# Kernel optimization log

Measured on AMD Instinct MI355X. Metric: run time of the kernel, lower is better.

Reference implementation:

```python
import jax, jax.numpy as jnp
import numpy as np

D = 2048  # d_model
B = 64    # batch
S = 32    # seq_len (module is designed for 32-step sequences)
C = 8     # number of control embeddings
INITRANGE = 0.1


def setup_inputs() -> dict:
    key = jax.random.key(0)
    ks = jax.random.split(key, 6)

    def lin_w(k):
        return jax.random.uniform(k, (D, D), minval=-INITRANGE, maxval=INITRANGE, dtype=jnp.float32)

    zb = jnp.zeros((D,), dtype=jnp.float32)
    return {
        "sequence": jax.random.normal(ks[0], (B, S, D), dtype=jnp.float32),
        "controls": jax.random.normal(ks[1], (C, B, D), dtype=jnp.float32),
        "Wq": lin_w(ks[2]), "bq": zb,
        "Wk": lin_w(ks[3]), "bk": zb,
        "Wv": lin_w(ks[4]), "bv": zb,
        "Wo": lin_w(ks[5]), "bo": zb,
    }


def reference(sequence, controls, Wq, bq, Wk, bk, Wv, bv, Wo, bo):
    # sequence: (B, S, D); controls: (C, B, D) = stacked list of control embeddings.
    d = sequence.shape[-1]
    queries = sequence @ Wq.T + bq            # (B, S, D)
    keys = controls @ Wk.T + bk               # (C, B, D)  == control_key(c).unsqueeze(1)
    values = controls @ Wv.T + bv             # (C, B, D)
    # bmm(queries, keys^T) with a single key per control -> scores (C, B, S, 1)
    scores = jnp.einsum('bsd,cbd->cbs', queries, keys)[..., None] / jnp.sqrt(jnp.asarray(d, sequence.dtype))
    attn = jax.nn.softmax(scores, axis=-1)    # softmax over a size-1 axis -> exactly 1.0
    attended = attn * values[:, :, None, :]   # (C, B, S, D); bmm(attn, values)
    # dropout is identity in eval mode
    projected = jnp.einsum('cbsd,ed->cbse', attended, Wo) + bo  # per-control output_proj
    # residual accumulation over the control loop == sum over C
    return sequence + projected.sum(axis=0)
```

## Files before the change

### kernel.cpp

```cpp
#include <hip/hip_runtime.h>
#include <hip/hip_bf16.h>

#define DM 2048
#define BB 64
#define SS 32
#define CC 8

typedef __attribute__((ext_vector_type(8))) short short8;
typedef __attribute__((ext_vector_type(4))) short short4v;
typedef __attribute__((ext_vector_type(4))) float f32x4;

static __device__ __forceinline__ short f2bf(float f) {
  union { __hip_bfloat16 h; short s; } u;
  u.h = __float2bfloat16(f);
  return u.s;
}

__global__ void k1_sum_bf16(const float* __restrict__ controls,
                            short* __restrict__ u16) {
  const int idx = blockIdx.x * 128 + threadIdx.x;
  const int b = idx >> 9;
  const int k = (idx & 511) * 4;
  float4 s = make_float4(0.f, 0.f, 0.f, 0.f);
#pragma unroll
  for (int c = 0; c < CC; ++c) {
    const float4 v = *reinterpret_cast<const float4*>(
        controls + ((size_t)c * BB + b) * DM + k);
    s.x += v.x; s.y += v.y; s.z += v.z; s.w += v.w;
  }
  short4v o = {f2bf(s.x), f2bf(s.y), f2bf(s.z), f2bf(s.w)};
  *reinterpret_cast<short4v*>(u16 + (size_t)b * DM + k) = o;
}

template <int EPI>
__global__ __launch_bounds__(512, 4) void gemm_full(
    const short* __restrict__ abf, const float* __restrict__ w,
    const float* __restrict__ bias, short* __restrict__ vout,
    const float* __restrict__ seq, float* __restrict__ out) {
  __shared__ float lwW[8][2][16 * 64];
  __shared__ f32x4 red[7][64];
  __shared__ float ptt[16][16];

  const int t    = threadIdx.x;
  const int lane = t & 63;
  const int wv   = t >> 6;
  const int eb   = blockIdx.x & 127;
  const int bg   = blockIdx.x >> 7;
  const int e0   = eb * 16;
  const int b0   = bg * 16;
  const int kq   = wv * 256;

  const int srow4 = lane >> 4;
  const int sg    = lane & 15;
  const int r = lane & 15, ksub = lane >> 4;

  const short* abase = abf + (size_t)(b0 + r) * DM + kq + ksub * 8;

  short8 areg[2][2];
  f32x4 acc = {0.f, 0.f, 0.f, 0.f};

#define ISSUE_W(c, bsel)                                                      \
  {                                                                           \
    const int ck = kq + (c) * 64;                                             \
    float* wd = &lwW[wv][bsel][0];                                            \
    _Pragma("unroll") for (int i = 0; i < 4; ++i) {                           \
      const int row = 4 * i + srow4;                                          \
      const float* src =                                                      \
          w + (size_t)(e0 + row) * DM + ck + ((sg ^ row) << 2);               \
      __builtin_amdgcn_global_load_lds(                                       \
          (const __attribute__((address_space(1))) void*)src,                 \
          (__attribute__((address_space(3))) void*)(wd + i * 256), 16, 0, 0); \
    }                                                                         \
  }
#define LOAD_A(c, bsel)                                                       \
  {                                                                           \
    areg[bsel][0] = *reinterpret_cast<const short8*>(abase + (c) * 64);       \
    areg[bsel][1] = *reinterpret_cast<const short8*>(abase + (c) * 64 + 32);  \
  }

  ISSUE_W(0, 0)
  LOAD_A(0, 0)

#pragma unroll
  for (int c = 0; c < 4; ++c) {
    if (c < 3) {
      ISSUE_W(c + 1, (c + 1) & 1)
      LOAD_A(c + 1, (c + 1) & 1)
      asm volatile("s_waitcnt vmcnt(6)" ::: "memory");
    } else {
      asm volatile("s_waitcnt vmcnt(0)" ::: "memory");
    }
    __builtin_amdgcn_sched_barrier(0);

    const float* wb = &lwW[wv][c & 1][0];
#pragma unroll
    for (int s = 0; s < 2; ++s) {
      const int gl = s * 8 + ksub * 2;
      const float4 lo =
          *reinterpret_cast<const float4*>(wb + r * 64 + ((gl ^ r) << 2));
      const float4 hi = *reinterpret_cast<const float4*>(
          wb + r * 64 + (((gl + 1) ^ r) << 2));
      short8 bf;
      bf[0] = f2bf(lo.x); bf[1] = f2bf(lo.y);
      bf[2] = f2bf(lo.z); bf[3] = f2bf(lo.w);
      bf[4] = f2bf(hi.x); bf[5] = f2bf(hi.y);
      bf[6] = f2bf(hi.z); bf[7] = f2bf(hi.w);
      acc = __builtin_amdgcn_mfma_f32_16x16x32_bf16(areg[c & 1][s], bf, acc,
                                                    0, 0, 0);
    }
  }
#undef ISSUE_W
#undef LOAD_A

  if (wv != 0) red[wv - 1][lane] = acc;
  __syncthreads();
  if (wv == 0) {
#pragma unroll
    for (int i = 0; i < 7; ++i) acc += red[i][lane];
    const float be = 8.f * bias[e0 + r];
    if (EPI == 0) {
#pragma unroll
      for (int j = 0; j < 4; ++j)
        vout[(size_t)(b0 + ksub * 4 + j) * DM + e0 + r] = f2bf(acc[j] + be);
    } else {
#pragma unroll
      for (int j = 0; j < 4; ++j) ptt[ksub * 4 + j][r] = acc[j] + be;
    }
  }

  if (EPI == 1) {
    __syncthreads();
    const int ef = (t & 3) * 4;
    const int sl = (t >> 2) & 7;
    const int bl = t >> 5;
    const float4 pv = *reinterpret_cast<const float4*>(&ptt[bl][ef]);
#pragma unroll
    for (int i = 0; i < 4; ++i) {
      const int s = sl + i * 8;
      const size_t off = ((size_t)(b0 + bl) * SS + s) * DM + e0 + ef;
      const float4 qd = *reinterpret_cast<const float4*>(seq + off);
      *reinterpret_cast<float4*>(out + off) =
          make_float4(qd.x + pv.x, qd.y + pv.y, qd.z + pv.z, qd.w + pv.w);
    }
  }
}

extern "C" void kernel_launch(void* const* d_in, const int* in_sizes, int n_in,
                              void* d_out, int out_size, void* d_ws,
                              size_t ws_size, hipStream_t stream) {
  const float* seq      = (const float*)d_in[0];
  const float* controls = (const float*)d_in[1];
  const float* Wv = (const float*)d_in[6];
  const float* bv = (const float*)d_in[7];
  const float* Wo = (const float*)d_in[8];
  const float* bo = (const float*)d_in[9];
  float* out = (float*)d_out;

  char* ws = (char*)d_ws;
  short* u16 = (short*)(ws);
  short* v16 = (short*)(ws + (512ull << 10));

  k1_sum_bf16<<<256, 128, 0, stream>>>(controls, u16);
  gemm_full<0><<<512, 512, 0, stream>>>(u16, Wv, bv, v16, nullptr, nullptr);
  gemm_full<1><<<512, 512, 0, stream>>>(v16, Wo, bo, nullptr, seq, out);
}
```

Baseline: 34.08 us.

## Split GEMM into specialized kernels with retuned K-splits and early seq prefetch

```diff
diff --git a/kernel.cpp b/kernel.cpp
--- a/kernel.cpp
+++ b/kernel.cpp
@@ -32,41 +32,35 @@
   *reinterpret_cast<short4v*>(u16 + (size_t)b * DM + k) = o;
 }
 
-template <int EPI>
-__global__ __launch_bounds__(512, 4) void gemm_full(
+__global__ __launch_bounds__(256, 2) void gemm_v16(
     const short* __restrict__ abf, const float* __restrict__ w,
-    const float* __restrict__ bias, short* __restrict__ vout,
-    const float* __restrict__ seq, float* __restrict__ out) {
-  __shared__ float lwW[8][2][16 * 64];
-  __shared__ f32x4 red[7][64];
-  __shared__ float ptt[16][16];
+    const float* __restrict__ bias, short* __restrict__ vout) {
+  __shared__ float lwW[4][2][16 * 128];
+  __shared__ f32x4 red[3][64];
 
   const int t    = threadIdx.x;
   const int lane = t & 63;
   const int wv   = t >> 6;
-  const int eb   = blockIdx.x & 127;
-  const int bg   = blockIdx.x >> 7;
-  const int e0   = eb * 16;
-  const int b0   = bg * 16;
-  const int kq   = wv * 256;
-
-  const int srow4 = lane >> 4;
-  const int sg    = lane & 15;
+  const int e0   = (blockIdx.x & 127) * 16;
+  const int b0   = (blockIdx.x >> 7) * 16;
+  const int kq   = wv * 512;
+
+  const int wrl = lane >> 5, wg = lane & 31;
   const int r = lane & 15, ksub = lane >> 4;
+  const int q = r & 7;
 
   const short* abase = abf + (size_t)(b0 + r) * DM + kq + ksub * 8;
-
-  short8 areg[2][2];
+  short8 areg[2][4];
   f32x4 acc = {0.f, 0.f, 0.f, 0.f};
 
 #define ISSUE_W(c, bsel)                                                      \
   {                                                                           \
-    const int ck = kq + (c) * 64;                                             \
+    const int ck = kq + (c) * 128;                                            \
     float* wd = &lwW[wv][bsel][0];                                            \
-    _Pragma("unroll") for (int i = 0; i < 4; ++i) {                           \
-      const int row = 4 * i + srow4;                                          \
+    _Pragma("unroll") for (int i = 0; i < 8; ++i) {                           \
+      const int row = 2 * i + wrl;                                            \
       const float* src =                                                      \
-          w + (size_t)(e0 + row) * DM + ck + ((sg ^ row) << 2);               \
+          w + (size_t)(e0 + row) * DM + ck + ((wg ^ (row & 7)) << 2);         \
       __builtin_amdgcn_global_load_lds(                                       \
           (const __attribute__((address_space(1))) void*)src,                 \
           (__attribute__((address_space(3))) void*)(wd + i * 256), 16, 0, 0); \
@@ -74,8 +68,8 @@
   }
 #define LOAD_A(c, bsel)                                                       \
   {                                                                           \
-    areg[bsel][0] = *reinterpret_cast<const short8*>(abase + (c) * 64);       \
-    areg[bsel][1] = *reinterpret_cast<const short8*>(abase + (c) * 64 + 32);  \
+    _Pragma("unroll") for (int s = 0; s < 4; ++s) areg[bsel][s] =             \
+        *reinterpret_cast<const short8*>(abase + (c) * 128 + s * 32);         \
   }
 
   ISSUE_W(0, 0)
@@ -86,9 +80,109 @@
     if (c < 3) {
       ISSUE_W(c + 1, (c + 1) & 1)
       LOAD_A(c + 1, (c + 1) & 1)
+      asm volatile("s_waitcnt vmcnt(12)" ::: "memory");
+    } else {
+      asm volatile("s_waitcnt vmcnt(0)" ::: "memory");
+    }
+    __builtin_amdgcn_sched_barrier(0);
+
+    const float* wb = &lwW[wv][c & 1][0];
+#pragma unroll
+    for (int s = 0; s < 4; ++s) {
+      const int gl = s * 8 + ksub * 2;
+      const float4 lo =
+          *reinterpret_cast<const float4*>(wb + r * 128 + ((gl ^ q) << 2));
+      const float4 hi = *reinterpret_cast<const float4*>(
+          wb + r * 128 + (((gl + 1) ^ q) << 2));
+      short8 bf;
+      bf[0] = f2bf(lo.x); bf[1] = f2bf(lo.y);
+      bf[2] = f2bf(lo.z); bf[3] = f2bf(lo.w);
+      bf[4] = f2bf(hi.x); bf[5] = f2bf(hi.y);
+      bf[6] = f2bf(hi.z); bf[7] = f2bf(hi.w);
+      acc = __builtin_amdgcn_mfma_f32_16x16x32_bf16(areg[c & 1][s], bf, acc,
+                                                    0, 0, 0);
+    }
+  }
+#undef ISSUE_W
+#undef LOAD_A
+
+  if (wv != 0) red[wv - 1][lane] = acc;
+  __syncthreads();
+  if (wv == 0) {
+#pragma unroll
+    for (int i = 0; i < 3; ++i) acc += red[i][lane];
+    const float be = 8.f * bias[e0 + r];
+#pragma unroll
+    for (int j = 0; j < 4; ++j)
+      vout[(size_t)(b0 + ksub * 4 + j) * DM + e0 + r] = f2bf(acc[j] + be);
+  }
+}
+
+__global__ __launch_bounds__(512, 2) void gemm_out(
+    const short* __restrict__ abf, const float* __restrict__ w,
+    const float* __restrict__ bias, const float* __restrict__ seq,
+    float* __restrict__ out) {
+  __shared__ float lwW[8][2][16 * 64];
+  __shared__ f32x4 red[2][3][64];
+  __shared__ float ptt[16][32];
+
+  const int t    = threadIdx.x;
+  const int lane = t & 63;
+  const int wv   = t >> 6;
+  const int eh   = wv & 1;
+  const int kqi  = wv >> 1;
+  const int e0   = (blockIdx.x & 63) * 32;
+  const int b0   = (blockIdx.x >> 6) * 16;
+  const int ew   = e0 + eh * 16;
+  const int kq   = kqi * 512;
+
+  const int rl4 = lane >> 4, g = lane & 15;
+  const int r = lane & 15, ksub = lane >> 4;
+
+  const short* abase = abf + (size_t)(b0 + r) * DM + kq + ksub * 8;
+  short8 areg[2][2];
+  f32x4 acc = {0.f, 0.f, 0.f, 0.f};
+
+  const int bl = t >> 5, rem = t & 31;
+  const int ef4 = (rem & 7) * 4, sl = rem >> 3;
+  float4 sreg[8];
+
+#define ISSUE_W2(c, bsel)                                                     \
+  {                                                                           \
+    const int ck = kq + (c) * 64;                                             \
+    float* wd = &lwW[wv][bsel][0];                                            \
+    _Pragma("unroll") for (int i = 0; i < 4; ++i) {                           \
+      const int row = 4 * i + rl4;                                            \
+      const float* src =                                                      \
+          w + (size_t)(ew + row) * DM + ck + ((g ^ row) << 2);                \
+      __builtin_amdgcn_global_load_lds(                                       \
+          (const __attribute__((address_space(1))) void*)src,                 \
+          (__attribute__((address_space(3))) void*)(wd + i * 256), 16, 0, 0); \
+    }                                                                         \
+  }
+#define LOAD_A2(c, bsel)                                                      \
+  {                                                                           \
+    areg[bsel][0] = *reinterpret_cast<const short8*>(abase + (c) * 64);       \
+    areg[bsel][1] = *reinterpret_cast<const short8*>(abase + (c) * 64 + 32);  \
+  }
+
+  ISSUE_W2(0, 0)
+  LOAD_A2(0, 0)
+
+#pragma unroll
+  for (int c = 0; c < 8; ++c) {
+    if (c < 7) {
+      ISSUE_W2(c + 1, (c + 1) & 1)
+      LOAD_A2(c + 1, (c + 1) & 1)
       asm volatile("s_waitcnt vmcnt(6)" ::: "memory");
     } else {
-      asm volatile("s_waitcnt vmcnt(0)" ::: "memory");
+#pragma unroll
+      for (int i = 0; i < 8; ++i) {
+        const size_t off =
+            ((size_t)(b0 + bl) * SS + (sl + 4 * i)) * DM + e0 + ef4;
+        sreg[i] = *reinterpret_cast<const float4*>(seq + off);
+      }
+      asm volatile("s_waitcnt vmcnt(8)" ::: "memory");
     }
     __builtin_amdgcn_sched_barrier(0);
 
@@ -109,39 +203,28 @@
                                                     0, 0, 0);
     }
   }
-#undef ISSUE_W
-#undef LOAD_A
-
-  if (wv != 0) red[wv - 1][lane] = acc;
+#undef ISSUE_W2
+#undef LOAD_A2
+
+  if (kqi != 0) red[eh][kqi - 1][lane] = acc;
   __syncthreads();
-  if (wv == 0) {
-#pragma unroll
-    for (int i = 0; i < 7; ++i) acc += red[i][lane];
-    const float be = 8.f * bias[e0 + r];
-    if (EPI == 0) {
-#pragma unroll
-      for (int j = 0; j < 4; ++j)
-        vout[(size_t)(b0 + ksub * 4 + j) * DM + e0 + r] = f2bf(acc[j] + be);
-    } else {
-#pragma unroll
-      for (int j = 0; j < 4; ++j) ptt[ksub * 4 + j][r] = acc[j] + be;
-    }
-  }
-
-  if (EPI == 1) {
-    __syncthreads();
-    const int ef = (t & 3) * 4;
-    const int sl = (t >> 2) & 7;
-    const int bl = t >> 5;
-    const float4 pv = *reinterpret_cast<const float4*>(&ptt[bl][ef]);
-#pragma unroll
-    for (int i = 0; i < 4; ++i) {
-      const int s = sl + i * 8;
-      const size_t off = ((size_t)(b0 + bl) * SS + s) * DM + e0 + ef;
-      const float4 qd = *reinterpret_cast<const float4*>(seq + off);
-      *reinterpret_cast<float4*>(out + off) =
-          make_float4(qd.x + pv.x, qd.y + pv.y, qd.z + pv.z, qd.w + pv.w);
-    }
+  if (kqi == 0) {
+#pragma unroll
+    for (int i = 0; i < 3; ++i) acc += red[eh][i][lane];
+    const float be = 8.f * bias[ew + r];
+#pragma unroll
+    for (int j = 0; j < 4; ++j) ptt[ksub * 4 + j][eh * 16 + r] = acc[j] + be;
+  }
+  __syncthreads();
+
+  const float4 pv = *reinterpret_cast<const float4*>(&ptt[bl][ef4]);
+  asm volatile("s_waitcnt vmcnt(0)" ::: "memory");
+#pragma unroll
+  for (int i = 0; i < 8; ++i) {
+    const size_t off = ((size_t)(b0 + bl) * SS + (sl + 4 * i)) * DM + e0 + ef4;
+    *reinterpret_cast<float4*>(out + off) =
+        make_float4(sreg[i].x + pv.x, sreg[i].y + pv.y, sreg[i].z + pv.z,
+                    sreg[i].w + pv.w);
   }
 }
 
@@ -161,6 +244,6 @@
   short* v16 = (short*)(ws + (512ull << 10));
 
   k1_sum_bf16<<<256, 128, 0, stream>>>(controls, u16);
-  gemm_full<0><<<512, 512, 0, stream>>>(u16, Wv, bv, v16, nullptr, nullptr);
-  gemm_full<1><<<512, 512, 0, stream>>>(v16, Wo, bo, nullptr, seq, out);
-}
+  gemm_v16<<<512, 256, 0, stream>>>(u16, Wv, bv, v16);
+  gemm_out<<<256, 512, 0, stream>>>(v16, Wo, bo, seq, out);
+}
```

After: 30.49 us. -10.5%, faster.
